# Performance work log

Hardware: AMD Instinct MI355X
Metric: run time of the kernel (lower is better)

The kernel has to match this reference:

```python
import jax, jax.numpy as jnp
import numpy as np

B, R, K_RANK = 128, 256, 10  # batch, rDim==cDim, rank
MU = 0.1
GAMMA = 0.51 * MU


def averaging_diagonals(X):
    """Project [..., m, n] matrices to Toeplitz by averaging each diagonal."""
    m, n = X.shape[-2:]
    # diagonal id for entry (i, j): j - i + (m - 1), in [0, m + n - 2]
    idx = (jnp.arange(n)[None, :] - jnp.arange(m)[:, None] + (m - 1)).reshape(-1)
    D = m + n - 1
    lead = X.shape[:-2]
    flat = X.reshape(lead + (m * n,))
    sums = jnp.zeros(lead + (D,), X.dtype).at[..., idx].add(flat)
    counts = jnp.zeros((D,), X.dtype).at[idx].add(jnp.ones((m * n,), X.dtype))
    avg = sums / counts
    return avg[..., idx].reshape(X.shape)


def rank_k(x, K):
    """Best rank-K approximation via truncated SVD, batched over leading dims."""
    U, S, Vh = jnp.linalg.svd(x, full_matrices=False)
    return jnp.einsum('...rk,...k,...kc->...rc', U[..., :K], S[..., :K], Vh[..., :K, :])


def setup_inputs() -> dict:
    key = jax.random.key(0)
    k1, k2, k3 = jax.random.split(key, 3)
    T = jax.random.normal(k1, (B, R, R), jnp.float32)
    Tp = jax.random.normal(k2, (B, R, R), jnp.float32)
    Sp = jax.random.normal(k3, (B, R, R), jnp.float32)
    # generateW: averagingDiagonals of indicator of first row/col
    S0 = jnp.zeros((R, R), jnp.float32).at[0, :].set(1.0).at[:, 0].set(1.0)
    W = averaging_diagonals(S0)
    w1 = jnp.eye(R, dtype=jnp.float32) * (1.0 - GAMMA)
    w2 = jnp.eye(R, dtype=jnp.float32) * GAMMA
    w3 = MU * W
    w4 = -MU * W
    return {"T": T, "Tp": Tp, "Sp": Sp, "w1": w1, "w2": w2, "w3": w3, "w4": w4, "K": K_RANK}


def reference(T, Tp, Sp, w1, w2, w3, w4, K):
    # Tptmp = w1 @ Sp + w2 @ Tp + w4 * Tp + w3 * T  (batched over B)
    Tptmp = (jnp.einsum('rk,bkc->brc', w1, Sp)
             + jnp.einsum('rk,bkc->brc', w2, Tp)
             + w4 * Tp + w3 * T)
    Tpnew = rank_k(Tptmp, K)
    Spnew = Sp - Tpnew + averaging_diagonals(2.0 * Tpnew - Sp)
    return (T, Tpnew, Spnew)
```

## Files before the change

### kernel.cpp

```cpp
#include <hip/hip_runtime.h>
#include <math.h>

#define B_   128
#define N_   256
#define L_   64
#define NRR  (N_*N_)
#define BRR  (B_*NRR)
#define BNL  (B_*N_*L_)

static __device__ __forceinline__ void fma4(float4& a, float s, const float4& v) {
  a.x += s * v.x; a.y += s * v.y; a.z += s * v.z; a.w += s * v.w;
}

__global__ __launch_bounds__(256) void k_build_A(
    const float* __restrict__ T, const float* __restrict__ Tp,
    const float* __restrict__ Sp, const float* __restrict__ w1,
    const float* __restrict__ w2, const float* __restrict__ w3,
    const float* __restrict__ w4, float* __restrict__ A) {
  int i4 = blockIdx.x * 256 + threadIdx.x;
  if (i4 >= BRR / 4) return;
  int rc4 = i4 & (NRR / 4 - 1);
  int r = rc4 >> 6;
  float a1 = w1[r * N_ + r], a2 = w2[r * N_ + r];
  float4 sp = ((const float4*)Sp)[i4];
  float4 tp = ((const float4*)Tp)[i4];
  float4 tt = ((const float4*)T)[i4];
  float4 w3v = ((const float4*)w3)[rc4];
  float4 w4v = ((const float4*)w4)[rc4];
  float4 o;
  o.x = a1 * sp.x + a2 * tp.x + w4v.x * tp.x + w3v.x * tt.x;
  o.y = a1 * sp.y + a2 * tp.y + w4v.y * tp.y + w3v.y * tt.y;
  o.z = a1 * sp.z + a2 * tp.z + w4v.z * tp.z + w3v.z * tt.z;
  o.w = a1 * sp.w + a2 * tp.w + w4v.w * tp.w + w3v.w * tt.w;
  ((float4*)A)[i4] = o;
}

__global__ __launch_bounds__(256) void k_aat(const float* __restrict__ A,
                                             float* __restrict__ G) {
  int b = blockIdx.z, ti = blockIdx.x, tj = blockIdx.y;
  if (ti > tj) return;
  int it = ti * 64, jt = tj * 64;
  __shared__ __align__(16) float AsT[32][68];
  __shared__ __align__(16) float BsT[32][68];
  const float* Ab = A + (size_t)b * NRR;
  int t = threadIdx.x, tx = t & 15, ty = t >> 4;
  float4 acc[4] = {};
  int kk = t & 31, r0 = t >> 5;
  for (int k0 = 0; k0 < N_; k0 += 32) {
#pragma unroll
    for (int p = 0; p < 8; ++p) {
      int r = r0 + p * 8;
      AsT[kk][r] = Ab[(it + r) * N_ + k0 + kk];
      BsT[kk][r] = Ab[(jt + r) * N_ + k0 + kk];
    }
    __syncthreads();
#pragma unroll
    for (int k = 0; k < 32; ++k) {
      float4 av = *(const float4*)&AsT[k][ty * 4];
      float4 bv = *(const float4*)&BsT[k][tx * 4];
      fma4(acc[0], av.x, bv);
      fma4(acc[1], av.y, bv);
      fma4(acc[2], av.z, bv);
      fma4(acc[3], av.w, bv);
    }
    __syncthreads();
  }
  float* Gb = G + (size_t)b * NRR;
#pragma unroll
  for (int i = 0; i < 4; ++i)
    *(float4*)&Gb[(it + ty * 4 + i) * N_ + jt + tx * 4] = acc[i];
  if (ti < tj) {
    const float* a = (const float*)acc;
#pragma unroll
    for (int i = 0; i < 4; ++i)
#pragma unroll
      for (int j = 0; j < 4; ++j)
        Gb[(jt + tx * 4 + j) * N_ + it + ty * 4 + i] = a[i * 4 + j];
  }
}

__global__ __launch_bounds__(128) void k_gq(const float* __restrict__ G,
                                            const float* __restrict__ Q,
                                            float* __restrict__ Y) {
  __shared__ __align__(16) float Qs[64][68];
  int b = blockIdx.y, it = blockIdx.x * 64;
  const float* Gb = G + (size_t)b * NRR;
  const float* Qb = Q + (size_t)b * (N_ * L_);
  int t = threadIdx.x, cx = t & 15, ry = t >> 4;
  const float* gr[8];
#pragma unroll
  for (int i = 0; i < 8; ++i) gr[i] = Gb + (size_t)(it + ry * 8 + i) * N_;
  float4 acc[8] = {};
  for (int kc = 0; kc < N_; kc += 64) {
#pragma unroll
    for (int p = 0; p < 8; ++p) {
      int idx = t + p * 128;
      int r = idx >> 4, c4 = idx & 15;
      *(float4*)&Qs[r][c4 * 4] = *(const float4*)&Qb[(kc + r) * L_ + c4 * 4];
    }
    __syncthreads();
#pragma unroll 4
    for (int k4 = 0; k4 < 16; ++k4) {
      int k = k4 * 4;
      float4 g[8];
#pragma unroll
      for (int i = 0; i < 8; ++i) g[i] = *(const float4*)&gr[i][kc + k];
      float4 q0 = *(const float4*)&Qs[k + 0][cx * 4];
      float4 q1 = *(const float4*)&Qs[k + 1][cx * 4];
      float4 q2 = *(const float4*)&Qs[k + 2][cx * 4];
      float4 q3 = *(const float4*)&Qs[k + 3][cx * 4];
#pragma unroll
      for (int i = 0; i < 8; ++i) {
        fma4(acc[i], g[i].x, q0);
        fma4(acc[i], g[i].y, q1);
        fma4(acc[i], g[i].z, q2);
        fma4(acc[i], g[i].w, q3);
      }
    }
    __syncthreads();
  }
  float* Yb = Y + (size_t)b * (N_ * L_);
#pragma unroll
  for (int i = 0; i < 8; ++i)
    *(float4*)&Yb[(it + ry * 8 + i) * L_ + cx * 4] = acc[i];
}

__global__ __launch_bounds__(256) void k_xty(const float* __restrict__ X,
                                             const float* __restrict__ Y,
                                             float* __restrict__ Mo) {
  int b = blockIdx.x, t = threadIdx.x, tx = t & 15, ty = t >> 4;
  const float* Xb = X + (size_t)b * (N_ * L_);
  const float* Yb = Y + (size_t)b * (N_ * L_);
  float4 a0 = {}, a1 = {}, a2 = {}, a3 = {};
#pragma unroll 4
  for (int k = 0; k < N_; ++k) {
    float4 xv = *(const float4*)&Xb[k * L_ + ty * 4];
    float4 yv = *(const float4*)&Yb[k * L_ + tx * 4];
    fma4(a0, xv.x, yv); fma4(a1, xv.y, yv);
    fma4(a2, xv.z, yv); fma4(a3, xv.w, yv);
  }
  float* Mb = Mo + (size_t)b * L_ * L_;
  *(float4*)&Mb[(ty * 4 + 0) * L_ + tx * 4] = a0;
  *(float4*)&Mb[(ty * 4 + 1) * L_ + tx * 4] = a1;
  *(float4*)&Mb[(ty * 4 + 2) * L_ + tx * 4] = a2;
  *(float4*)&Mb[(ty * 4 + 3) * L_ + tx * 4] = a3;
}

__global__ __launch_bounds__(256) void k_init_Y(float* __restrict__ Y) {
  int idx = blockIdx.x * 256 + threadIdx.x;
  if (idx >= BNL) return;
  unsigned u = (unsigned)idx * 2654435761u;
  u ^= u >> 16; u *= 2246822519u; u ^= u >> 13; u *= 3266489917u; u ^= u >> 16;
  Y[idx] = (float)(int)u * 4.6566129e-10f;
}

__global__ __launch_bounds__(256) void k_qr(float* __restrict__ Q) {
  __shared__ __align__(16) float S[64][68];
  __shared__ float dinv[64];
  int b = blockIdx.x, t = threadIdx.x, tx = t & 15, ty = t >> 4;
  float* Qb = Q + (size_t)b * (N_ * L_);
  {
    float4 a0 = {}, a1 = {}, a2 = {}, a3 = {};
#pragma unroll 4
    for (int k = 0; k < N_; ++k) {
      float4 xv = *(const float4*)&Qb[k * L_ + ty * 4];
      float4 yv = *(const float4*)&Qb[k * L_ + tx * 4];
      fma4(a0, xv.x, yv); fma4(a1, xv.y, yv);
      fma4(a2, xv.z, yv); fma4(a3, xv.w, yv);
    }
    *(float4*)&S[ty * 4 + 0][tx * 4] = a0;
    *(float4*)&S[ty * 4 + 1][tx * 4] = a1;
    *(float4*)&S[ty * 4 + 2][tx * 4] = a2;
    *(float4*)&S[ty * 4 + 3][tx * 4] = a3;
  }
  __syncthreads();
  for (int kb = 0; kb < 8; ++kb) {
    int base = kb * 8;
    if (t == 0) {
      for (int q = 0; q < 8; ++q) {
        float d = S[base + q][base + q];
        for (int w = 0; w < q; ++w) d -= S[base + q][base + w] * S[base + q][base + w];
        d = sqrtf(fmaxf(d, 1e-20f));
        S[base + q][base + q] = d;
        float di = 1.f / d;
        dinv[base + q] = di;
        for (int r = q + 1; r < 8; ++r) {
          float v = S[base + r][base + q];
          for (int w = 0; w < q; ++w) v -= S[base + r][base + w] * S[base + q][base + w];
          S[base + r][base + q] = v * di;
        }
      }
    }
    __syncthreads();
    int nrows = 56 - base;
    if (t < nrows) {
      int i = base + 8 + t;
      float x[8];
#pragma unroll
      for (int q = 0; q < 8; ++q) {
        float v = S[i][base + q];
        for (int w = 0; w < q; ++w) v -= S[base + q][base + w] * x[w];
        x[q] = v * dinv[base + q];
      }
#pragma unroll
      for (int q = 0; q < 8; ++q) S[i][base + q] = x[q];
    }
    __syncthreads();
    if (nrows > 0) {
      for (int e = t; e < nrows * 64; e += 256) {
        int io = e >> 6, ko = e & 63;
        if (ko < nrows) {
          int i = base + 8 + io, k = base + 8 + ko;
          float4 p0 = *(const float4*)&S[i][base], p1 = *(const float4*)&S[i][base + 4];
          float4 r0 = *(const float4*)&S[k][base], r1 = *(const float4*)&S[k][base + 4];
          S[i][k] -= p0.x * r0.x + p0.y * r0.y + p0.z * r0.z + p0.w * r0.w
                   + p1.x * r1.x + p1.y * r1.y + p1.z * r1.z + p1.w * r1.w;
        }
      }
    }
    __syncthreads();
  }
  {
    float x[64];
#pragma unroll
    for (int u = 0; u < 16; ++u) {
      float4 v = *(const float4*)&Qb[t * L_ + u * 4];
      x[u * 4 + 0] = v.x; x[u * 4 + 1] = v.y;
      x[u * 4 + 2] = v.z; x[u * 4 + 3] = v.w;
    }
#pragma unroll
    for (int j = 0; j < 64; ++j) {
      float s = x[j];
#pragma unroll
      for (int mq = 0; mq < (j >> 2); ++mq) {
        float4 lv = *(const float4*)&S[j][mq * 4];
        s -= lv.x * x[mq * 4 + 0] + lv.y * x[mq * 4 + 1]
           + lv.z * x[mq * 4 + 2] + lv.w * x[mq * 4 + 3];
      }
#pragma unroll
      for (int k = (j & ~3); k < j; ++k) s -= S[j][k] * x[k];
      x[j] = s * dinv[j];
    }
#pragma unroll
    for (int u = 0; u < 16; ++u) {
      float4 v;
      v.x = x[u * 4 + 0]; v.y = x[u * 4 + 1];
      v.z = x[u * 4 + 2]; v.w = x[u * 4 + 3];
      *(float4*)&Qb[t * L_ + u * 4] = v;
    }
  }
}

__global__ __launch_bounds__(256) void k_jacobi(float* __restrict__ Mg,
                                                float* __restrict__ Vg) {
  __shared__ __align__(16) float A[64][68];
  __shared__ __align__(16) float Vt[64][68];
  int b = blockIdx.x, t = threadIdx.x;
  float* Mb = Mg + (size_t)b * L_ * L_;
#pragma unroll
  for (int p = 0; p < 16; ++p) {
    int e = t + p * 256, r = e >> 6, c = e & 63;
    A[r][c] = Mb[r * L_ + c];
    Vt[r][c] = (r == c) ? 1.f : 0.f;
  }
  __syncthreads();
  int m = t >> 3, u = t & 7;
  for (int sweep = 0; sweep < 4; ++sweep) {
    for (int rnd = 0; rnd < 63; ++rnd) {
      int i, j;
      if (m == 0) { i = rnd; j = 63; }
      else {
        int a = rnd + m;       if (a >= 63) a -= 63;
        int bb = rnd + 63 - m; if (bb >= 63) bb -= 63;
        i = min(a, bb); j = max(a, bb);
      }
      float aii = A[i][i], ajj = A[j][j], aij = A[i][j];
      float c_ = 1.f, s_ = 0.f;
      if (fabsf(aij) > 1e-12f) {
        float tau = (ajj - aii) / (2.f * aij);
        float tt = (tau >= 0.f ? 1.f : -1.f) / (fabsf(tau) + sqrtf(1.f + tau * tau));
        c_ = rsqrtf(1.f + tt * tt);
        s_ = tt * c_;
      }
      {
        float4* Ai = (float4*)&A[i][u * 8];
        float4* Aj = (float4*)&A[j][u * 8];
        float4* Vi = (float4*)&Vt[i][u * 8];
        float4* Vj = (float4*)&Vt[j][u * 8];
#pragma unroll
        for (int q = 0; q < 2; ++q) {
          float4 x = Ai[q], y = Aj[q], nx, ny;
          nx.x = c_ * x.x - s_ * y.x; ny.x = s_ * x.x + c_ * y.x;
          nx.y = c_ * x.y - s_ * y.y; ny.y = s_ * x.y + c_ * y.y;
          nx.z = c_ * x.z - s_ * y.z; ny.z = s_ * x.z + c_ * y.z;
          nx.w = c_ * x.w - s_ * y.w; ny.w = s_ * x.w + c_ * y.w;
          Ai[q] = nx; Aj[q] = ny;
          float4 vx = Vi[q], vy = Vj[q], mx, my;
          mx.x = c_ * vx.x - s_ * vy.x; my.x = s_ * vx.x + c_ * vy.x;
          mx.y = c_ * vx.y - s_ * vy.y; my.y = s_ * vx.y + c_ * vy.y;
          mx.z = c_ * vx.z - s_ * vy.z; my.z = s_ * vx.z + c_ * vy.z;
          mx.w = c_ * vx.w - s_ * vy.w; my.w = s_ * vx.w + c_ * vy.w;
          Vi[q] = mx; Vj[q] = my;
        }
      }
      __syncthreads();
#pragma unroll
      for (int p = 0; p < 8; ++p) {
        int k = u + 8 * p;
        float x = A[k][i], y = A[k][j];
        A[k][i] = c_ * x - s_ * y;
        A[k][j] = s_ * x + c_ * y;
      }
      __syncthreads();
    }
  }
  if (t < 64) Mb[t * L_ + t] = A[t][t];
  float* Vb = Vg + (size_t)b * L_ * L_;
#pragma unroll
  for (int p = 0; p < 16; ++p) {
    int e = t + p * 256, r = e >> 6, c = e & 63;
    Vb[r * L_ + c] = Vt[r][c];
  }
}

__global__ void k_topk(const float* __restrict__ Mg, const int* __restrict__ Kp,
                       int* __restrict__ topidx) {
  int b = blockIdx.x;
  if (threadIdx.x != 0) return;
  const float* Mb = Mg + (size_t)b * L_ * L_;
  int K = *Kp; if (K > 16) K = 16;
  float vals[64]; bool used[64];
  for (int i = 0; i < 64; ++i) { vals[i] = Mb[i * L_ + i]; used[i] = false; }
  for (int j = 0; j < K; ++j) {
    int best = 0; float bv = -1e30f;
    for (int i = 0; i < 64; ++i)
      if (!used[i] && vals[i] > bv) { bv = vals[i]; best = i; }
    used[best] = true;
    topidx[b * 16 + j] = best;
  }
}

__global__ __launch_bounds__(256) void k_formU(const float* __restrict__ Q,
                                               const float* __restrict__ Vtg,
                                               const int* __restrict__ topidx,
                                               const int* __restrict__ Kp,
                                               float* __restrict__ U) {
  __shared__ float Vs[64][17];
  int b = blockIdx.x, t = threadIdx.x;
  int K = *Kp; if (K > 16) K = 16;
  if (t < 64) {
    for (int j = 0; j < 16; ++j)
      Vs[t][j] = (j < K)
        ? Vtg[(size_t)b * L_ * L_ + (size_t)topidx[b * 16 + j] * L_ + t]
        : 0.f;
  }
  __syncthreads();
  const float* Qb = Q + (size_t)b * N_ * L_;
  float qv[64];
#pragma unroll
  for (int k = 0; k < 64; ++k) qv[k] = Qb[t * L_ + k];
  float* Ub = U + (size_t)b * N_ * 16;
  for (int j = 0; j < 16; ++j) {
    float s = 0.f;
    if (j < K) {
#pragma unroll
      for (int k = 0; k < 64; ++k) s += qv[k] * Vs[k][j];
    }
    Ub[t * 16 + j] = s;
  }
}

__global__ __launch_bounds__(256) void k_utA(const float* __restrict__ U,
                                             const float* __restrict__ A,
                                             const int* __restrict__ Kp,
                                             float* __restrict__ C) {
  __shared__ float Us[256][17];
  int b = blockIdx.x, t = threadIdx.x;
  int K = *Kp; if (K > 16) K = 16;
  const float* Ub = U + (size_t)b * N_ * 16;
  for (int p = 0; p < 16; ++p) {
    int r = (t >> 4) + p * 16, j = t & 15;
    Us[r][j] = Ub[r * 16 + j];
  }
  __syncthreads();
  const float* Ab = A + (size_t)b * NRR;
  float acc[16];
  for (int j = 0; j < 16; ++j) acc[j] = 0.f;
  for (int i = 0; i < N_; ++i) {
    float av = Ab[i * N_ + t];
    for (int j = 0; j < K; ++j) acc[j] += Us[i][j] * av;
  }
  float* Cb = C + (size_t)b * 16 * N_;
  for (int j = 0; j < 16; ++j) Cb[j * N_ + t] = (j < K) ? acc[j] : 0.f;
}

__global__ __launch_bounds__(256) void k_uc(const float* __restrict__ U,
                                            const float* __restrict__ C,
                                            const int* __restrict__ Kp,
                                            float* __restrict__ Tpnew) {
  __shared__ float Cs[16][256];
  __shared__ float Us[16][17];
  int b = blockIdx.y, rt = blockIdx.x * 16, t = threadIdx.x;
  int K = *Kp; if (K > 16) K = 16;
  const float* Cb = C + (size_t)b * 16 * N_;
  for (int j = 0; j < 16; ++j) Cs[j][t] = Cb[j * N_ + t];
  Us[t >> 4][t & 15] = U[(size_t)b * N_ * 16 + (size_t)(rt + (t >> 4)) * 16 + (t & 15)];
  __syncthreads();
  float* Ob = Tpnew + (size_t)b * NRR;
  for (int r = 0; r < 16; ++r) {
    float s = 0.f;
    for (int j = 0; j < K; ++j) s += Us[r][j] * Cs[j][t];
    Ob[(rt + r) * N_ + t] = s;
  }
}

__global__ __launch_bounds__(256) void k_copyT(const float* __restrict__ T,
                                               float* __restrict__ O) {
  int i4 = blockIdx.x * 256 + threadIdx.x;
  if (i4 < BRR / 4) ((float4*)O)[i4] = ((const float4*)T)[i4];
}

__global__ __launch_bounds__(256) void k_spnew(const float* __restrict__ Sp,
                                               const float* __restrict__ Tpnew,
                                               float* __restrict__ Spnew) {
  __shared__ float sums[512];
  int b = blockIdx.x, t = threadIdx.x;
  for (int i = t; i < 512; i += 256) sums[i] = 0.f;
  __syncthreads();
  const float4* Spb = (const float4*)(Sp + (size_t)b * NRR);
  const float4* Tb  = (const float4*)(Tpnew + (size_t)b * NRR);
  for (int i4 = t; i4 < NRR / 4; i4 += 256) {
    int r = i4 >> 6, c = (i4 & 63) * 4;
    float4 tv = Tb[i4], sv = Spb[i4];
    int d = c - r + 255;
    atomicAdd(&sums[d + 0], 2.f * tv.x - sv.x);
    atomicAdd(&sums[d + 1], 2.f * tv.y - sv.y);
    atomicAdd(&sums[d + 2], 2.f * tv.z - sv.z);
    atomicAdd(&sums[d + 3], 2.f * tv.w - sv.w);
  }
  __syncthreads();
  for (int d = t; d < 511; d += 256) {
    int cnt = 256 - (d < 255 ? 255 - d : d - 255);
    sums[d] /= (float)cnt;
  }
  __syncthreads();
  float4* Ob = (float4*)(Spnew + (size_t)b * NRR);
  for (int i4 = t; i4 < NRR / 4; i4 += 256) {
    int r = i4 >> 6, c = (i4 & 63) * 4;
    float4 tv = Tb[i4], sv = Spb[i4];
    int d = c - r + 255;
    float4 o;
    o.x = sv.x - tv.x + sums[d + 0];
    o.y = sv.y - tv.y + sums[d + 1];
    o.z = sv.z - tv.z + sums[d + 2];
    o.w = sv.w - tv.w + sums[d + 3];
    Ob[i4] = o;
  }
}

extern "C" void kernel_launch(void* const* d_in, const int* in_sizes, int n_in,
                              void* d_out, int out_size, void* d_ws, size_t ws_size,
                              hipStream_t stream) {
  const float* T  = (const float*)d_in[0];
  const float* Tp = (const float*)d_in[1];
  const float* Sp = (const float*)d_in[2];
  const float* w1 = (const float*)d_in[3];
  const float* w2 = (const float*)d_in[4];
  const float* w3 = (const float*)d_in[5];
  const float* w4 = (const float*)d_in[6];
  const int*   Kp = (const int*)d_in[7];
  float* out = (float*)d_out;

  float* slot0 = out;
  float* slot1 = out + BRR;
  float* slot2 = out + 2 * (size_t)BRR;
  float* G = slot0;
  float* A = slot1;
  float* Qb[2] = { slot2, slot2 + BNL };
  float* sc    = slot2 + 2 * (size_t)BNL;
  float* Mbuf  = sc;
  float* Vbuf  = sc + 524288;
  float* Ubuf  = sc + 2 * 524288;
  float* Cbuf  = sc + 3 * 524288;
  int*   topidx = (int*)(sc + 4 * 524288);

  k_build_A<<<BRR / 4 / 256, 256, 0, stream>>>(T, Tp, Sp, w1, w2, w3, w4, A);
  k_aat<<<dim3(4, 4, B_), 256, 0, stream>>>(A, G);
  k_init_Y<<<BNL / 256, 256, 0, stream>>>(Qb[0]);
  k_qr<<<B_, 256, 0, stream>>>(Qb[0]);

  int cur = 0;
  for (int it = 0; it < 12; ++it) {
    k_gq<<<dim3(4, B_), 128, 0, stream>>>(G, Qb[cur], Qb[1 - cur]);
    cur = 1 - cur;
    if ((it & 3) == 3) k_qr<<<B_, 256, 0, stream>>>(Qb[cur]);
  }
  k_gq<<<dim3(4, B_), 128, 0, stream>>>(G, Qb[cur], Qb[1 - cur]);
  k_xty<<<B_, 256, 0, stream>>>(Qb[cur], Qb[1 - cur], Mbuf);
  k_jacobi<<<B_, 256, 0, stream>>>(Mbuf, Vbuf);
  k_topk<<<B_, 64, 0, stream>>>(Mbuf, Kp, topidx);
  k_formU<<<B_, 256, 0, stream>>>(Qb[cur], Vbuf, topidx, Kp, Ubuf);
  k_utA<<<B_, 256, 0, stream>>>(Ubuf, A, Kp, Cbuf);
  k_uc<<<dim3(16, B_), 256, 0, stream>>>(Ubuf, Cbuf, Kp, slot1);
  k_copyT<<<BRR / 4 / 256, 256, 0, stream>>>(T, slot0);
  k_spnew<<<B_, 256, 0, stream>>>(Sp, slot1, slot2);
}
```

Before: 1.537 ms.

## Double-buffer Jacobi with 2x2 block rotations and widen gq to 256 threads

The Jacobi eigen-solver now uses 512 threads and two copies of A in shared memory. Each thread applies the combined left and right rotations to 2x2 blocks in one step, halving the number of block barriers per rotation round. The G·Q power-iteration kernel moves to 256 threads with 4 rows per thread instead of 8, raising parallelism per block at the cost of more Q tile loads per row. The extra shared buffer raises LDS use, and the joint rotation slightly changes the floating-point ordering.

Result: faster. 1.497 ms (-2.6%).

```diff
diff --git a/kernel.cpp b/kernel.cpp
--- a/kernel.cpp
+++ b/kernel.cpp
@@ -79,7 +79,7 @@
   }
 }
 
-__global__ __launch_bounds__(128) void k_gq(const float* __restrict__ G,
+__global__ __launch_bounds__(256) void k_gq(const float* __restrict__ G,
                                             const float* __restrict__ Q,
                                             float* __restrict__ Y) {
   __shared__ __align__(16) float Qs[64][68];
@@ -87,14 +87,14 @@
   const float* Gb = G + (size_t)b * NRR;
   const float* Qb = Q + (size_t)b * (N_ * L_);
   int t = threadIdx.x, cx = t & 15, ry = t >> 4;
-  const float* gr[8];
-#pragma unroll
-  for (int i = 0; i < 8; ++i) gr[i] = Gb + (size_t)(it + ry * 8 + i) * N_;
-  float4 acc[8] = {};
+  const float* gr[4];
+#pragma unroll
+  for (int i = 0; i < 4; ++i) gr[i] = Gb + (size_t)(it + ry * 4 + i) * N_;
+  float4 acc[4] = {};
   for (int kc = 0; kc < N_; kc += 64) {
 #pragma unroll
-    for (int p = 0; p < 8; ++p) {
-      int idx = t + p * 128;
+    for (int p = 0; p < 4; ++p) {
+      int idx = t + p * 256;
       int r = idx >> 4, c4 = idx & 15;
       *(float4*)&Qs[r][c4 * 4] = *(const float4*)&Qb[(kc + r) * L_ + c4 * 4];
     }
@@ -102,15 +102,15 @@
 #pragma unroll 4
     for (int k4 = 0; k4 < 16; ++k4) {
       int k = k4 * 4;
-      float4 g[8];
-#pragma unroll
-      for (int i = 0; i < 8; ++i) g[i] = *(const float4*)&gr[i][kc + k];
+      float4 g[4];
+#pragma unroll
+      for (int i = 0; i < 4; ++i) g[i] = *(const float4*)&gr[i][kc + k];
       float4 q0 = *(const float4*)&Qs[k + 0][cx * 4];
       float4 q1 = *(const float4*)&Qs[k + 1][cx * 4];
       float4 q2 = *(const float4*)&Qs[k + 2][cx * 4];
       float4 q3 = *(const float4*)&Qs[k + 3][cx * 4];
 #pragma unroll
-      for (int i = 0; i < 8; ++i) {
+      for (int i = 0; i < 4; ++i) {
         fma4(acc[i], g[i].x, q0);
         fma4(acc[i], g[i].y, q1);
         fma4(acc[i], g[i].z, q2);
@@ -121,8 +121,8 @@
   }
   float* Yb = Y + (size_t)b * (N_ * L_);
 #pragma unroll
-  for (int i = 0; i < 8; ++i)
-    *(float4*)&Yb[(it + ry * 8 + i) * L_ + cx * 4] = acc[i];
+  for (int i = 0; i < 4; ++i)
+    *(float4*)&Yb[(it + ry * 4 + i) * L_ + cx * 4] = acc[i];
 }
 
 __global__ __launch_bounds__(256) void k_xty(const float* __restrict__ X,
@@ -251,74 +251,91 @@
   }
 }
 
-__global__ __launch_bounds__(256) void k_jacobi(float* __restrict__ Mg,
+static __device__ __forceinline__ void pair_of(int rnd, int g, int& i, int& j) {
+  if (g == 0) { i = rnd; j = 63; }
+  else {
+    int a = rnd + g;       if (a >= 63) a -= 63;
+    int bb = rnd + 63 - g; if (bb >= 63) bb -= 63;
+    i = a < bb ? a : bb; j = a < bb ? bb : a;
+  }
+}
+
+static __device__ __forceinline__ void jparams(float (*Ac)[68], int i, int j,
+                                               float& c_, float& s_) {
+  float aii = Ac[i][i], ajj = Ac[j][j], aij = Ac[i][j];
+  c_ = 1.f; s_ = 0.f;
+  if (fabsf(aij) > 1e-12f) {
+    float tau = (ajj - aii) / (2.f * aij);
+    float tt = (tau >= 0.f ? 1.f : -1.f) / (fabsf(tau) + sqrtf(1.f + tau * tau));
+    c_ = rsqrtf(1.f + tt * tt);
+    s_ = tt * c_;
+  }
+}
+
+__global__ __launch_bounds__(512) void k_jacobi(float* __restrict__ Mg,
                                                 float* __restrict__ Vg) {
-  __shared__ __align__(16) float A[64][68];
+  __shared__ __align__(16) float A[2][64][68];
   __shared__ __align__(16) float Vt[64][68];
   int b = blockIdx.x, t = threadIdx.x;
   float* Mb = Mg + (size_t)b * L_ * L_;
 #pragma unroll
-  for (int p = 0; p < 16; ++p) {
-    int e = t + p * 256, r = e >> 6, c = e & 63;
-    A[r][c] = Mb[r * L_ + c];
+  for (int p = 0; p < 8; ++p) {
+    int e = t + p * 512, r = e >> 6, c = e & 63;
+    A[0][r][c] = Mb[r * L_ + c];
     Vt[r][c] = (r == c) ? 1.f : 0.f;
   }
   __syncthreads();
-  int m = t >> 3, u = t & 7;
+  int m = t >> 4, u = t & 15;
+  int q0 = 2 * u, q1 = 2 * u + 1;
+  int cur = 0;
   for (int sweep = 0; sweep < 4; ++sweep) {
     for (int rnd = 0; rnd < 63; ++rnd) {
-      int i, j;
-      if (m == 0) { i = rnd; j = 63; }
-      else {
-        int a = rnd + m;       if (a >= 63) a -= 63;
-        int bb = rnd + 63 - m; if (bb >= 63) bb -= 63;
-        i = min(a, bb); j = max(a, bb);
-      }
-      float aii = A[i][i], ajj = A[j][j], aij = A[i][j];
-      float c_ = 1.f, s_ = 0.f;
-      if (fabsf(aij) > 1e-12f) {
-        float tau = (ajj - aii) / (2.f * aij);
-        float tt = (tau >= 0.f ? 1.f : -1.f) / (fabsf(tau) + sqrtf(1.f + tau * tau));
-        c_ = rsqrtf(1.f + tt * tt);
-        s_ = tt * c_;
-      }
+      float (*Ac)[68] = A[cur];
+      float (*An)[68] = A[cur ^ 1];
+      int i, j, k0, l0, k1, l1;
+      pair_of(rnd, m, i, j);
+      pair_of(rnd, q0, k0, l0);
+      pair_of(rnd, q1, k1, l1);
+      float c0, s0, cA, sA, cB, sB;
+      jparams(Ac, i, j, c0, s0);
+      jparams(Ac, k0, l0, cA, sA);
+      jparams(Ac, k1, l1, cB, sB);
       {
-        float4* Ai = (float4*)&A[i][u * 8];
-        float4* Aj = (float4*)&A[j][u * 8];
-        float4* Vi = (float4*)&Vt[i][u * 8];
-        float4* Vj = (float4*)&Vt[j][u * 8];
-#pragma unroll
-        for (int q = 0; q < 2; ++q) {
-          float4 x = Ai[q], y = Aj[q], nx, ny;
-          nx.x = c_ * x.x - s_ * y.x; ny.x = s_ * x.x + c_ * y.x;
-          nx.y = c_ * x.y - s_ * y.y; ny.y = s_ * x.y + c_ * y.y;
-          nx.z = c_ * x.z - s_ * y.z; ny.z = s_ * x.z + c_ * y.z;
-          nx.w = c_ * x.w - s_ * y.w; ny.w = s_ * x.w + c_ * y.w;
-          Ai[q] = nx; Aj[q] = ny;
-          float4 vx = Vi[q], vy = Vj[q], mx, my;
-          mx.x = c_ * vx.x - s_ * vy.x; my.x = s_ * vx.x + c_ * vy.x;
-          mx.y = c_ * vx.y - s_ * vy.y; my.y = s_ * vx.y + c_ * vy.y;
-          mx.z = c_ * vx.z - s_ * vy.z; my.z = s_ * vx.z + c_ * vy.z;
-          mx.w = c_ * vx.w - s_ * vy.w; my.w = s_ * vx.w + c_ * vy.w;
-          Vi[q] = mx; Vj[q] = my;
-        }
+        float aik = Ac[i][k0], ail = Ac[i][l0];
+        float ajk = Ac[j][k0], ajl = Ac[j][l0];
+        float bik = c0 * aik - s0 * ajk, bjk = s0 * aik + c0 * ajk;
+        float bil = c0 * ail - s0 * ajl, bjl = s0 * ail + c0 * ajl;
+        An[i][k0] = cA * bik - sA * bil; An[i][l0] = sA * bik + cA * bil;
+        An[j][k0] = cA * bjk - sA * bjl; An[j][l0] = sA * bjk + cA * bjl;
+      }
+      {
+        float aik = Ac[i][k1], ail = Ac[i][l1];
+        float ajk = Ac[j][k1], ajl = Ac[j][l1];
+        float bik = c0 * aik - s0 * ajk, bjk = s0 * aik + c0 * ajk;
+        float bil = c0 * ail - s0 * ajl, bjl = s0 * ail + c0 * ajl;
+        An[i][k1] = cB * bik - sB * bil; An[i][l1] = sB * bik + cB * bil;
+        An[j][k1] = cB * bjk - sB * bjl; An[j][l1] = sB * bjk + cB * bjl;
+      }
+      {
+        float4 vi = *(const float4*)&Vt[i][u * 4];
+        float4 vj = *(const float4*)&Vt[j][u * 4];
+        float4 ni, nj;
+        ni.x = c0 * vi.x - s0 * vj.x; nj.x = s0 * vi.x + c0 * vj.x;
+        ni.y = c0 * vi.y - s0 * vj.y; nj.y = s0 * vi.y + c0 * vj.y;
+        ni.z = c0 * vi.z - s0 * vj.z; nj.z = s0 * vi.z + c0 * vj.z;
+        ni.w = c0 * vi.w - s0 * vj.w; nj.w = s0 * vi.w + c0 * vj.w;
+        *(float4*)&Vt[i][u * 4] = ni;
+        *(float4*)&Vt[j][u * 4] = nj;
       }
       __syncthreads();
-#pragma unroll
-      for (int p = 0; p < 8; ++p) {
-        int k = u + 8 * p;
-        float x = A[k][i], y = A[k][j];
-        A[k][i] = c_ * x - s_ * y;
-        A[k][j] = s_ * x + c_ * y;
-      }
-      __syncthreads();
-    }
-  }
-  if (t < 64) Mb[t * L_ + t] = A[t][t];
+      cur ^= 1;
+    }
+  }
+  if (t < 64) Mb[t * L_ + t] = A[cur][t][t];
   float* Vb = Vg + (size_t)b * L_ * L_;
 #pragma unroll
-  for (int p = 0; p < 16; ++p) {
-    int e = t + p * 256, r = e >> 6, c = e & 63;
+  for (int p = 0; p < 8; ++p) {
+    int e = t + p * 512, r = e >> 6, c = e & 63;
     Vb[r * L_ + c] = Vt[r][c];
   }
 }
@@ -491,13 +508,13 @@
 
   int cur = 0;
   for (int it = 0; it < 12; ++it) {
-    k_gq<<<dim3(4, B_), 128, 0, stream>>>(G, Qb[cur], Qb[1 - cur]);
+    k_gq<<<dim3(4, B_), 256, 0, stream>>>(G, Qb[cur], Qb[1 - cur]);
     cur = 1 - cur;
     if ((it & 3) == 3) k_qr<<<B_, 256, 0, stream>>>(Qb[cur]);
   }
-  k_gq<<<dim3(4, B_), 128, 0, stream>>>(G, Qb[cur], Qb[1 - cur]);
+  k_gq<<<dim3(4, B_), 256, 0, stream>>>(G, Qb[cur], Qb[1 - cur]);
   k_xty<<<B_, 256, 0, stream>>>(Qb[cur], Qb[1 - cur], Mbuf);
-  k_jacobi<<<B_, 256, 0, stream>>>(Mbuf, Vbuf);
+  k_jacobi<<<B_, 512, 0, stream>>>(Mbuf, Vbuf);
   k_topk<<<B_, 64, 0, stream>>>(Mbuf, Kp, topidx);
   k_formU<<<B_, 256, 0, stream>>>(Qb[cur], Vbuf, topidx, Kp, Ubuf);
   k_utA<<<B_, 256, 0, stream>>>(Ubuf, A, Kp, Cbuf);
```
